# Optimization experiments

Hardware: AMD Instinct MI355X
Metric: run time of the kernel (lower is better)

Reference implementation:

```python
import jax, jax.numpy as jnp
import numpy as np


def gcn_conv(x, src, dst, deg_inv_sqrt, W, b):
    # PyG GCNConv: h = x @ W, then symmetric-normalized scatter-add over edges
    # (edge list already includes self-loops; deg computed over it).
    h = x @ W                                   # [N, F_out]
    norm = deg_inv_sqrt[src] * deg_inv_sqrt[dst]  # [E]
    msgs = h[src] * norm[:, None]               # gather + scale
    out = jax.ops.segment_sum(msgs, dst, num_segments=x.shape[0])
    return out + b


def setup_inputs() -> dict:
    key = jax.random.key(0)
    k1, k2, k3, k4 = jax.random.split(key, 4)
    N, E, F_in, F_hid, F_out = 200000, 6400000, 128, 8, 16
    x = jax.random.normal(k1, (N, F_in), dtype=jnp.float32)
    edge_index = jax.random.randint(k2, (2, E), 0, N, dtype=jnp.int64)
    W1 = jax.random.normal(k3, (F_in, F_hid), dtype=jnp.float32) * (1.0 / np.sqrt(F_in))
    b1 = jnp.zeros((F_hid,), dtype=jnp.float32)
    W2 = jax.random.normal(k4, (F_hid, F_out), dtype=jnp.float32) * (1.0 / np.sqrt(F_hid))
    b2 = jnp.zeros((F_out,), dtype=jnp.float32)
    return {"x": x, "edge_index": edge_index, "W1": W1, "b1": b1, "W2": W2, "b2": b2}


def reference(x, edge_index, W1, b1, W2, b2):
    N = x.shape[0]
    # add self-loops (GCNConv default add_self_loops=True)
    loops = jnp.arange(N, dtype=edge_index.dtype)
    src = jnp.concatenate([edge_index[0], loops])
    dst = jnp.concatenate([edge_index[1], loops])
    deg = jax.ops.segment_sum(jnp.ones_like(dst, dtype=x.dtype), dst, num_segments=N)
    deg_inv_sqrt = jnp.where(deg > 0, jax.lax.rsqrt(deg), 0.0)
    h = jax.nn.relu(gcn_conv(x, src, dst, deg_inv_sqrt, W1, b1))
    # dropout is identity in eval mode (training=False)
    out = gcn_conv(h, src, dst, deg_inv_sqrt, W2, b2)
    return out
```

## Files before the change

### kernel.cpp

```cpp
#include <hip/hip_runtime.h>
#include <hip/hip_fp16.h>

#define F_IN  128
#define F_HID 8
#define F_OUT 16

#define SBSH  9
#define SBW   (1 << SBSH)
#define MAXB  400
#define BIN_CAP  32
#define FLUSH_G  16


typedef float f32x4 __attribute__((ext_vector_type(4)));
typedef int   i32x4 __attribute__((ext_vector_type(4)));

__global__ __launch_bounds__(512) void stage_bin(const int* __restrict__ ei,
                                                 int* __restrict__ gcur,
                                                 int* __restrict__ stage,
                                                 int E, int B, int cap, int per_block) {
    __shared__ int bin_cnt[MAXB];
    __shared__ int bin_buf[MAXB * BIN_CAP];
    for (int i = threadIdx.x; i < B; i += blockDim.x) bin_cnt[i] = 0;
    __syncthreads();
    const bool vec = ((E & 3) == 0);
    int base = blockIdx.x * per_block;
    int end  = min(E, base + per_block);
    for (int it = base; it < end; it += (int)blockDim.x * 4) {
        int e = it + (int)threadIdx.x * 4;
        int sv[4], dv[4], m4 = 0;
        if (vec && e + 3 < end) {
            i32x4 s4 = __builtin_nontemporal_load((const i32x4*)(ei + e));
            i32x4 d4 = __builtin_nontemporal_load((const i32x4*)(ei + E + e));
            sv[0] = s4.x; sv[1] = s4.y; sv[2] = s4.z; sv[3] = s4.w;
            dv[0] = d4.x; dv[1] = d4.y; dv[2] = d4.z; dv[3] = d4.w;
            m4 = 4;
        } else {
            for (int q = 0; e + q < end && q < 4; q++) { sv[q] = ei[e + q]; dv[q] = ei[E + e + q]; m4++; }
        }
        for (int q = 0; q < m4; q++) {
            int b   = dv[q] >> SBSH;
            int val = (sv[q] << SBSH) | (dv[q] & (SBW - 1));
            int pos = atomicAdd(&bin_cnt[b], 1);
            if (pos < BIN_CAP) {
                bin_buf[b * BIN_CAP + ((pos + b) & (BIN_CAP - 1))] = val;
            } else {
                int gp = b * cap + atomicAdd(&gcur[b], 1);
                stage[gp] = val;
            }
        }
        __syncthreads();
        for (int b2 = threadIdx.x; b2 < B; b2 += blockDim.x) {
            int c = min(bin_cnt[b2], BIN_CAP);
            while (c >= FLUSH_G) {
                int s0 = c - FLUSH_G;
                int r  = b2 * cap + atomicAdd(&gcur[b2], FLUSH_G);
#pragma unroll
                for (int k = 0; k < FLUSH_G; k++)
                    stage[r + k] = bin_buf[b2 * BIN_CAP + ((s0 + k + b2) & (BIN_CAP - 1))];
                c = s0;
            }
            bin_cnt[b2] = c;
        }
        __syncthreads();
    }
    for (int b2 = threadIdx.x; b2 < B; b2 += blockDim.x) {
        int c = min(bin_cnt[b2], BIN_CAP);
        if (c > 0) {
            int r = b2 * cap + atomicAdd(&gcur[b2], c);
            for (int k = 0; k < c; k++)
                stage[r + k] = bin_buf[b2 * BIN_CAP + ((k + b2) & (BIN_CAP - 1))];
        }
    }
}

__global__ __launch_bounds__(1024) void scatter_csr(const int* __restrict__ stage,
                                                    const int* __restrict__ gcur,
                                                    int cap,
                                                    int* __restrict__ cnt,
                                                    float* __restrict__ dis,
                                                    int* __restrict__ row_start,
                                                    int* __restrict__ csr, int n) {
    __shared__ int s0[SBW], s1[SBW];
    int b  = blockIdx.x;
    int nb = b << SBSH;
    int i  = threadIdx.x;
    if (i < SBW) s0[i] = 0;
    __syncthreads();
    int base = b * cap;
    int num  = gcur[b];
    for (int k = i; k < num; k += 1024)
        atomicAdd(&s0[stage[base + k] & (SBW - 1)], 1);
    __syncthreads();
    int c = (i < SBW) ? s0[i] : 0;
    if (i < SBW && nb + i < n) { cnt[nb + i] = c; dis[nb + i] = rsqrtf((float)(c + 1)); }
    int* src = s0; int* dst = s1;
    for (int off = 1; off < SBW; off <<= 1) {
        if (i < SBW) dst[i] = src[i] + ((i >= off) ? src[i - off] : 0);
        __syncthreads();
        int* t = src; src = dst; dst = t;
    }
    if (i < SBW) {
        int e = base + src[i] - c;
        if (nb + i < n) row_start[nb + i] = e;
        dst[i] = e;
    }
    __syncthreads();
    for (int k = i; k < num; k += 1024) {
        int v = stage[base + k];
        int pos = atomicAdd(&dst[v & (SBW - 1)], 1);
        csr[pos] = v >> SBSH;
    }
}

__global__ __launch_bounds__(256) void gemm1(const float* __restrict__ x,
                                             const float* __restrict__ W1,
                                             const float* __restrict__ dis,
                                             __half* __restrict__ g1, int n) {
    __shared__ float w2[F_HID * F_IN];
    for (int i = threadIdx.x; i < F_HID * F_IN; i += blockDim.x) {
        int f = i >> 7, k = i & (F_IN - 1);
        w2[i] = W1[k * F_HID + f];
    }
    __syncthreads();
    int t = blockIdx.x * blockDim.x + threadIdx.x;
    int node = t >> 3, l = t & 7;
    if (node >= n) return;
    const f32x4* xr = (const f32x4*)(x + (size_t)node * F_IN);
    float acc[F_HID];
#pragma unroll
    for (int f = 0; f < F_HID; f++) acc[f] = 0.0f;
#pragma unroll
    for (int it = 0; it < 4; it++) {
        int j = l + it * 8;
        f32x4 v = __builtin_nontemporal_load(xr + j);
#pragma unroll
        for (int f = 0; f < F_HID; f++) {
            const float* wf = &w2[f * F_IN + j * 4];
            acc[f] += v[0] * wf[0] + v[1] * wf[1] + v[2] * wf[2] + v[3] * wf[3];
        }
    }
#pragma unroll
    for (int f = 0; f < F_HID; f++) {
        acc[f] += __shfl_xor(acc[f], 1);
        acc[f] += __shfl_xor(acc[f], 2);
        acc[f] += __shfl_xor(acc[f], 4);
    }
    if (l == 0) {
        float d = dis[node];
        __half2 h[4];
#pragma unroll
        for (int p = 0; p < 4; p++) h[p] = __floats2half2_rn(acc[2 * p] * d, acc[2 * p + 1] * d);
        *(uint4*)(g1 + (size_t)node * F_HID) = *(uint4*)h;
    }
}

__global__ __launch_bounds__(256) void aggregate_relu(const int* __restrict__ csr,
                                                      const int* __restrict__ row_start,
                                                      const int* __restrict__ cnt,
                                                      const float* __restrict__ dis,
                                                      const float* __restrict__ b1,
                                                      const __half* __restrict__ gin,
                                                      __half* __restrict__ gout, int n) {
    int t = blockIdx.x * blockDim.x + threadIdx.x;
    int node = t >> 2;
    int l = t & 3;
    if (node >= n) return;
    const __half2* g2 = (const __half2*)gin;
    int beg = row_start[node];
    int c   = cnt[node];
    float2 acc = __half22float2(g2[(unsigned)node * 4 + l]);
    int j = 0;
    int cm8 = c & ~7;
    for (; j < cm8; j += 8) {
        int va = __builtin_nontemporal_load(csr + beg + j + l);
        int vb = __builtin_nontemporal_load(csr + beg + j + 4 + l);
        int s0 = __shfl(va, 0, 4), s1 = __shfl(va, 1, 4);
        int s2 = __shfl(va, 2, 4), s3 = __shfl(va, 3, 4);
        int s4 = __shfl(vb, 0, 4), s5 = __shfl(vb, 1, 4);
        int s6 = __shfl(vb, 2, 4), s7 = __shfl(vb, 3, 4);
        __half2 h0 = g2[(unsigned)s0 * 4 + l];
        __half2 h1 = g2[(unsigned)s1 * 4 + l];
        __half2 h2 = g2[(unsigned)s2 * 4 + l];
        __half2 h3 = g2[(unsigned)s3 * 4 + l];
        __half2 h4 = g2[(unsigned)s4 * 4 + l];
        __half2 h5 = g2[(unsigned)s5 * 4 + l];
        __half2 h6 = g2[(unsigned)s6 * 4 + l];
        __half2 h7 = g2[(unsigned)s7 * 4 + l];
        float2 f0 = __half22float2(h0), f1 = __half22float2(h1);
        float2 f2 = __half22float2(h2), f3 = __half22float2(h3);
        float2 f4 = __half22float2(h4), f5 = __half22float2(h5);
        float2 f6 = __half22float2(h6), f7 = __half22float2(h7);
        acc.x += ((f0.x + f1.x) + (f2.x + f3.x)) + ((f4.x + f5.x) + (f6.x + f7.x));
        acc.y += ((f0.y + f1.y) + (f2.y + f3.y)) + ((f4.y + f5.y) + (f6.y + f7.y));
    }
    for (; j < c; j++) {
        int s = __builtin_nontemporal_load(csr + beg + j);
        float2 a = __half22float2(g2[(unsigned)s * 4 + l]);
        acc.x += a.x; acc.y += a.y;
    }
    float d = dis[node];
    float2 bv = *(const float2*)(b1 + 2 * l);
    float rx = fmaxf(fmaf(acc.x, d, bv.x), 0.0f) * d;
    float ry = fmaxf(fmaf(acc.y, d, bv.y), 0.0f) * d;
    ((__half2*)gout)[(unsigned)node * 4 + l] = __floats2half2_rn(rx, ry);
}

__global__ __launch_bounds__(256) void aggregate_out(const int* __restrict__ csr,
                                                     const int* __restrict__ row_start,
                                                     const int* __restrict__ cnt,
                                                     const float* __restrict__ dis,
                                                     const float* __restrict__ W2,
                                                     const float* __restrict__ b2,
                                                     const __half* __restrict__ gin,
                                                     float* __restrict__ out, int n) {
    int t = blockIdx.x * blockDim.x + threadIdx.x;
    int node = t >> 2;
    int l = t & 3;
    if (node >= n) return;
    const __half2* g2 = (const __half2*)gin;
    int beg = row_start[node];
    int c   = cnt[node];
    float2 acc = __half22float2(g2[(unsigned)node * 4 + l]);
    int j = 0;
    int cm8 = c & ~7;
    for (; j < cm8; j += 8) {
        int va = __builtin_nontemporal_load(csr + beg + j + l);
        int vb = __builtin_nontemporal_load(csr + beg + j + 4 + l);
        int s0 = __shfl(va, 0, 4), s1 = __shfl(va, 1, 4);
        int s2 = __shfl(va, 2, 4), s3 = __shfl(va, 3, 4);
        int s4 = __shfl(vb, 0, 4), s5 = __shfl(vb, 1, 4);
        int s6 = __shfl(vb, 2, 4), s7 = __shfl(vb, 3, 4);
        __half2 h0 = g2[(unsigned)s0 * 4 + l];
        __half2 h1 = g2[(unsigned)s1 * 4 + l];
        __half2 h2 = g2[(unsigned)s2 * 4 + l];
        __half2 h3 = g2[(unsigned)s3 * 4 + l];
        __half2 h4 = g2[(unsigned)s4 * 4 + l];
        __half2 h5 = g2[(unsigned)s5 * 4 + l];
        __half2 h6 = g2[(unsigned)s6 * 4 + l];
        __half2 h7 = g2[(unsigned)s7 * 4 + l];
        float2 f0 = __half22float2(h0), f1 = __half22float2(h1);
        float2 f2 = __half22float2(h2), f3 = __half22float2(h3);
        float2 f4 = __half22float2(h4), f5 = __half22float2(h5);
        float2 f6 = __half22float2(h6), f7 = __half22float2(h7);
        acc.x += ((f0.x + f1.x) + (f2.x + f3.x)) + ((f4.x + f5.x) + (f6.x + f7.x));
        acc.y += ((f0.y + f1.y) + (f2.y + f3.y)) + ((f4.y + f5.y) + (f6.y + f7.y));
    }
    for (; j < c; j++) {
        int s = __builtin_nontemporal_load(csr + beg + j);
        float2 a = __half22float2(g2[(unsigned)s * 4 + l]);
        acc.x += a.x; acc.y += a.y;
    }
    float d = dis[node];
    float ax = acc.x * d, ay = acc.y * d;
    float4 o = ((const float4*)b2)[l];
#pragma unroll
    for (int s = 0; s < 4; s++) {
        float axs = __shfl(ax, s, 4);
        float ays = __shfl(ay, s, 4);
        float4 w0 = ((const float4*)W2)[(2 * s) * 4 + l];
        float4 w1 = ((const float4*)W2)[(2 * s + 1) * 4 + l];
        o.x = fmaf(axs, w0.x, fmaf(ays, w1.x, o.x));
        o.y = fmaf(axs, w0.y, fmaf(ays, w1.y, o.y));
        o.z = fmaf(axs, w0.z, fmaf(ays, w1.z, o.z));
        o.w = fmaf(axs, w0.w, fmaf(ays, w1.w, o.w));
    }
    *(float4*)(out + (size_t)node * F_OUT + 4 * l) = o;
}

extern "C" void kernel_launch(void* const* d_in, const int* in_sizes, int n_in,
                              void* d_out, int out_size, void* d_ws, size_t ws_size,
                              hipStream_t stream) {
    const float* x  = (const float*)d_in[0];
    const int*   ei = (const int*)d_in[1];
    const float* W1 = (const float*)d_in[2];
    const float* b1 = (const float*)d_in[3];
    const float* W2 = (const float*)d_in[4];
    const float* b2 = (const float*)d_in[5];
    float* out = (float*)d_out;

    const int N = in_sizes[0] / F_IN;
    const int E = in_sizes[1] / 2;
    const int B = (N + SBW - 1) >> SBSH;

    int avg = (E + B - 1) / B;
    int cap = (avg + avg / 16 + 255) & ~255;

    int*    stage     = (int*)d_ws;
    int*    csr       = stage + (size_t)B * cap;
    float*  dis       = (float*)(csr + (size_t)B * cap);
    __half* gA        = (__half*)(dis + N);
    __half* gB        = (__half*)((int*)gA + (size_t)N * 4);
    int*    cnt       = (int*)gB + (size_t)N * 4;
    int*    row_start = cnt + N;
    int*    gcur      = row_start + N;

    const int BT = 256;
    dim3 thr(BT);
    dim3 blkG(((size_t)N * 8 + BT - 1) / BT);
    dim3 blkA(((size_t)N * 4 + BT - 1) / BT);

    int per_block = ((E + 639) / 640 + 2047) & ~2047;
    int SBLK = (E + per_block - 1) / per_block;

    hipMemsetAsync(gcur, 0, (size_t)B * sizeof(int), stream);
    stage_bin     <<<dim3(SBLK), dim3(512), 0, stream>>>(ei, gcur, stage, E, B, cap, per_block);
    scatter_csr   <<<dim3(B),   dim3(1024), 0, stream>>>(stage, gcur, cap, cnt, dis, row_start, csr, N);
    gemm1         <<<blkG, thr, 0, stream>>>(x, W1, dis, gA, N);
    aggregate_relu<<<blkA, thr, 0, stream>>>(csr, row_start, cnt, dis, b1, gA, gB, N);
    aggregate_out <<<blkA, thr, 0, stream>>>(csr, row_start, cnt, dis, W2, b2, gB, out, N);
}
```

Before: 436.9 us.

## Fuse CSR scatter with first-layer GEMM and cache staged edges in registers

Merges the CSR-building kernel with the x@W1 GEMM, so each 512-node bucket block also computes its nodes' hidden features, using degree scales kept in shared memory. Each thread now holds up to 17 staged edge values in registers, so the stage buffer is read once rather than twice across the count and scatter passes. The final output store becomes nontemporal. In exchange, the large per-thread register array may lower occupancy of the 1024-thread blocks, and the GEMM now runs on only B blocks, which may limit the parallelism available for streaming x.

```diff
diff --git a/kernel.cpp b/kernel.cpp
--- a/kernel.cpp
+++ b/kernel.cpp
@@ -10,6 +10,7 @@
 #define MAXB  400
 #define BIN_CAP  32
 #define FLUSH_G  16
+#define RPT   17
 
 
 typedef float f32x4 __attribute__((ext_vector_type(4)));
@@ -74,26 +75,49 @@
     }
 }
 
-__global__ __launch_bounds__(1024) void scatter_csr(const int* __restrict__ stage,
-                                                    const int* __restrict__ gcur,
-                                                    int cap,
-                                                    int* __restrict__ cnt,
-                                                    float* __restrict__ dis,
-                                                    int* __restrict__ row_start,
-                                                    int* __restrict__ csr, int n) {
-    __shared__ int s0[SBW], s1[SBW];
+__global__ __launch_bounds__(1024) void build_gemm(const int* __restrict__ stage,
+                                                   const int* __restrict__ gcur,
+                                                   int cap,
+                                                   const float* __restrict__ x,
+                                                   const float* __restrict__ W1,
+                                                   int* __restrict__ cnt,
+                                                   float* __restrict__ dis,
+                                                   int* __restrict__ row_start,
+                                                   int* __restrict__ csr,
+                                                   __half* __restrict__ g1, int n) {
+    __shared__ int   s0[SBW], s1[SBW];
+    __shared__ float w2[F_HID * F_IN];
+    __shared__ float disl[SBW];
     int b  = blockIdx.x;
     int nb = b << SBSH;
     int i  = threadIdx.x;
+    if (i < F_HID * F_IN) {
+        int f = i >> 7, k = i & (F_IN - 1);
+        w2[i] = W1[k * F_HID + f];
+    }
     if (i < SBW) s0[i] = 0;
     __syncthreads();
     int base = b * cap;
     int num  = gcur[b];
-    for (int k = i; k < num; k += 1024)
+    int rv[RPT];
+#pragma unroll
+    for (int q = 0; q < RPT; q++) {
+        int k = i + q * 1024;
+        rv[q] = (k < num) ? stage[base + k] : -1;
+    }
+#pragma unroll
+    for (int q = 0; q < RPT; q++)
+        if (rv[q] >= 0) atomicAdd(&s0[rv[q] & (SBW - 1)], 1);
+    for (int k = RPT * 1024 + i; k < num; k += 1024)
         atomicAdd(&s0[stage[base + k] & (SBW - 1)], 1);
     __syncthreads();
     int c = (i < SBW) ? s0[i] : 0;
-    if (i < SBW && nb + i < n) { cnt[nb + i] = c; dis[nb + i] = rsqrtf((float)(c + 1)); }
+    if (i < SBW && nb + i < n) {
+        cnt[nb + i] = c;
+        float dv = rsqrtf((float)(c + 1));
+        dis[nb + i] = dv;
+        disl[i] = dv;
+    }
     int* src = s0; int* dst = s1;
     for (int off = 1; off < SBW; off <<= 1) {
         if (i < SBW) dst[i] = src[i] + ((i >= off) ? src[i - off] : 0);
@@ -106,52 +130,53 @@
         dst[i] = e;
     }
     __syncthreads();
-    for (int k = i; k < num; k += 1024) {
+#pragma unroll
+    for (int q = 0; q < RPT; q++) {
+        if (rv[q] >= 0) {
+            int v = rv[q];
+            int pos = atomicAdd(&dst[v & (SBW - 1)], 1);
+            csr[pos] = v >> SBSH;
+        }
+    }
+    for (int k = RPT * 1024 + i; k < num; k += 1024) {
         int v = stage[base + k];
         int pos = atomicAdd(&dst[v & (SBW - 1)], 1);
         csr[pos] = v >> SBSH;
     }
-}
-
-__global__ __launch_bounds__(256) void gemm1(const float* __restrict__ x,
-                                             const float* __restrict__ W1,
-                                             const float* __restrict__ dis,
-                                             __half* __restrict__ g1, int n) {
-    __shared__ float w2[F_HID * F_IN];
-    for (int i = threadIdx.x; i < F_HID * F_IN; i += blockDim.x) {
-        int f = i >> 7, k = i & (F_IN - 1);
-        w2[i] = W1[k * F_HID + f];
-    }
-    __syncthreads();
-    int t = blockIdx.x * blockDim.x + threadIdx.x;
-    int node = t >> 3, l = t & 7;
-    if (node >= n) return;
-    const f32x4* xr = (const f32x4*)(x + (size_t)node * F_IN);
-    float acc[F_HID];
-#pragma unroll
-    for (int f = 0; f < F_HID; f++) acc[f] = 0.0f;
-#pragma unroll
-    for (int it = 0; it < 4; it++) {
-        int j = l + it * 8;
-        f32x4 v = __builtin_nontemporal_load(xr + j);
+    __syncthreads();
+    int g = i >> 3, l = i & 7;
+#pragma unroll
+    for (int j = 0; j < 4; j++) {
+        int ln   = j * 128 + g;
+        int node = nb + ln;
+        if (node >= n) continue;
+        const f32x4* xr = (const f32x4*)(x + (size_t)node * F_IN);
+        float acc[F_HID];
+#pragma unroll
+        for (int f = 0; f < F_HID; f++) acc[f] = 0.0f;
+#pragma unroll
+        for (int it = 0; it < 4; it++) {
+            int jj = l + it * 8;
+            f32x4 v = __builtin_nontemporal_load(xr + jj);
+#pragma unroll
+            for (int f = 0; f < F_HID; f++) {
+                const float* wf = &w2[f * F_IN + jj * 4];
+                acc[f] += v[0] * wf[0] + v[1] * wf[1] + v[2] * wf[2] + v[3] * wf[3];
+            }
+        }
 #pragma unroll
         for (int f = 0; f < F_HID; f++) {
-            const float* wf = &w2[f * F_IN + j * 4];
-            acc[f] += v[0] * wf[0] + v[1] * wf[1] + v[2] * wf[2] + v[3] * wf[3];
-        }
-    }
-#pragma unroll
-    for (int f = 0; f < F_HID; f++) {
-        acc[f] += __shfl_xor(acc[f], 1);
-        acc[f] += __shfl_xor(acc[f], 2);
-        acc[f] += __shfl_xor(acc[f], 4);
-    }
-    if (l == 0) {
-        float d = dis[node];
-        __half2 h[4];
-#pragma unroll
-        for (int p = 0; p < 4; p++) h[p] = __floats2half2_rn(acc[2 * p] * d, acc[2 * p + 1] * d);
-        *(uint4*)(g1 + (size_t)node * F_HID) = *(uint4*)h;
+            acc[f] += __shfl_xor(acc[f], 1);
+            acc[f] += __shfl_xor(acc[f], 2);
+            acc[f] += __shfl_xor(acc[f], 4);
+        }
+        if (l == 0) {
+            float d = disl[ln];
+            __half2 h[4];
+#pragma unroll
+            for (int p = 0; p < 4; p++) h[p] = __floats2half2_rn(acc[2 * p] * d, acc[2 * p + 1] * d);
+            *(uint4*)(g1 + (size_t)node * F_HID) = *(uint4*)h;
+        }
     }
 }
 
@@ -265,7 +290,8 @@
         o.z = fmaf(axs, w0.z, fmaf(ays, w1.z, o.z));
         o.w = fmaf(axs, w0.w, fmaf(ays, w1.w, o.w));
     }
-    *(float4*)(out + (size_t)node * F_OUT + 4 * l) = o;
+    f32x4 ov = {o.x, o.y, o.z, o.w};
+    __builtin_nontemporal_store(ov, (f32x4*)(out + (size_t)node * F_OUT + 4 * l));
 }
 
 extern "C" void kernel_launch(void* const* d_in, const int* in_sizes, int n_in,
@@ -297,7 +323,6 @@
 
     const int BT = 256;
     dim3 thr(BT);
-    dim3 blkG(((size_t)N * 8 + BT - 1) / BT);
     dim3 blkA(((size_t)N * 4 + BT - 1) / BT);
 
     int per_block = ((E + 639) / 640 + 2047) & ~2047;
@@ -305,8 +330,8 @@
 
     hipMemsetAsync(gcur, 0, (size_t)B * sizeof(int), stream);
     stage_bin     <<<dim3(SBLK), dim3(512), 0, stream>>>(ei, gcur, stage, E, B, cap, per_block);
-    scatter_csr   <<<dim3(B),   dim3(1024), 0, stream>>>(stage, gcur, cap, cnt, dis, row_start, csr, N);
-    gemm1         <<<blkG, thr, 0, stream>>>(x, W1, dis, gA, N);
+    build_gemm    <<<dim3(B), dim3(1024), 0, stream>>>(stage, gcur, cap, x, W1,
+                                                       cnt, dis, row_start, csr, gA, N);
     aggregate_relu<<<blkA, thr, 0, stream>>>(csr, row_start, cnt, dis, b1, gA, gB, N);
     aggregate_out <<<blkA, thr, 0, stream>>>(csr, row_start, cnt, dis, W2, b2, gB, out, N);
 }
```

New measurement: 419.8 us. 3.9% less time.
